# Optimization experiments

Measured on AMD Instinct MI355X. Metric: run time of the kernel, lower is better.

The kernel has to match this reference:

```python
import jax, jax.numpy as jnp
import numpy as np

B, T, C, H = 2, 2048, 1024, 16
HD = C // H  # head dim = 64


def setup_inputs() -> dict:
    key = jax.random.key(0)
    k1, k2, k3 = jax.random.split(key, 3)
    x = jax.random.normal(k1, (B, T, C), dtype=jnp.float32)
    W_attn = jax.random.normal(k2, (C, 3 * C), dtype=jnp.float32) * (C ** -0.5)
    W_proj = jax.random.normal(k3, (C, C), dtype=jnp.float32) * (C ** -0.5)
    b_proj = jnp.zeros((C,), dtype=jnp.float32)
    return {"x": x, "W_attn": W_attn, "W_proj": W_proj, "b_proj": b_proj}


def reference(x, W_attn, W_proj, b_proj):
    Bv, Tv, Cv = x.shape
    qkv = x @ W_attn  # [B, T, 3C]  (no bias: config.bias=False)
    # NOTE: source splits as k, q, v (k first!)
    k, q, v = jnp.split(qkv, 3, axis=2)
    # [B, H, T, HD]
    q = q.reshape(Bv, Tv, H, HD).transpose(0, 2, 1, 3)
    k = k.reshape(Bv, Tv, H, HD).transpose(0, 2, 1, 3)
    v = v.reshape(Bv, Tv, H, HD).transpose(0, 2, 1, 3)
    wei = jnp.einsum('bhqd,bhkd->bhqk', q, k) * (HD ** -0.5)
    causal = jnp.tril(jnp.ones((Tv, Tv), dtype=bool))
    wei = jnp.where(causal, wei, -jnp.inf)
    wei = jax.nn.softmax(wei, axis=-1)
    # dropout = 0.0 (eval) -> identity
    out = jnp.einsum('bhqk,bhkd->bhqd', wei, v)
    out = out.transpose(0, 2, 1, 3).reshape(Bv, Tv, Cv)
    out = out @ W_proj + b_proj
    return out
```

## Files before the change

kernel.cpp:

```cpp
#include <hip/hip_runtime.h>

typedef __attribute__((ext_vector_type(8))) short short8;
typedef __attribute__((ext_vector_type(4))) short short4v;
typedef __attribute__((ext_vector_type(4))) float float4v;

#define T_SEQ 2048
#define CDIM 1024
#define NHEAD 16
#define HDIM 64
#define PROW 72

__device__ __forceinline__ unsigned short f2bf(float f) {
    unsigned u = __builtin_bit_cast(unsigned, f);
    u += 0x7FFF + ((u >> 16) & 1);
    return (unsigned short)(u >> 16);
}

__device__ __forceinline__ void gload16(const unsigned short* g,
                                        unsigned short* l) {
    __builtin_amdgcn_global_load_lds(
        (const __attribute__((address_space(1))) unsigned int*)g,
        (__attribute__((address_space(3))) unsigned int*)l, 16, 0, 0);
}

__device__ __forceinline__ void phase_barrier() {
    __builtin_amdgcn_sched_barrier(0);
    __builtin_amdgcn_s_barrier();
    __builtin_amdgcn_sched_barrier(0);
}

__global__ __launch_bounds__(256) void preproc(
    const float* __restrict__ x, unsigned short* __restrict__ xb,
    const float* __restrict__ Wa, unsigned short* __restrict__ WaT,
    const float* __restrict__ Wp, unsigned short* __restrict__ WpT) {
    int bid = blockIdx.x, tid = threadIdx.x;
    if (bid < 4096) {
        int i = bid * 256 + tid;
        float4 v = ((const float4*)x)[i];
        ushort4 o;
        o.x = f2bf(v.x); o.y = f2bf(v.y); o.z = f2bf(v.z); o.w = f2bf(v.w);
        ((ushort4*)xb)[i] = o;
        return;
    }
    __shared__ float tile[32][33];
    const float* in;
    unsigned short* out;
    int N, b;
    if (bid < 4096 + 3072) {
        b = bid - 4096; in = Wa; out = WaT; N = 3072;
    } else {
        b = bid - 7168; in = Wp; out = WpT; N = 1024;
    }
    const int K = 1024;
    int kb = (b & 31) * 32, nb = (b >> 5) * 32;
    int tx = tid & 31, ty = tid >> 5;
    for (int r = 0; r < 4; r++)
        tile[ty + r * 8][tx] = in[(size_t)(kb + ty + r * 8) * N + nb + tx];
    __syncthreads();
    for (int r = 0; r < 4; r++)
        out[(size_t)(nb + ty + r * 8) * K + kb + tx] = f2bf(tile[tx][ty + r * 8]);
}

__global__ __launch_bounds__(256) void gemm_qkv(
    const unsigned short* __restrict__ A, const unsigned short* __restrict__ Bt,
    unsigned short* __restrict__ dK, unsigned short* __restrict__ dQ,
    unsigned short* __restrict__ dV) {
    const int K = 1024;
    const int NITER = K / 32;
    __shared__ unsigned short sA[3][128 * 32];
    __shared__ unsigned short sB[3][128 * 32];
    int tid = threadIdx.x, wave = tid >> 6, lane = tid & 63;
    int quad = lane >> 4, l16 = lane & 15;
    int wm = wave >> 1, wn = wave & 1;
    int blockM = blockIdx.y * 128, blockN = blockIdx.x * 128;
    bool swapAB = (blockN >= 2048);

    const unsigned short* gA = A + (size_t)blockM * K;
    const unsigned short* gB = Bt + (size_t)blockN * K;

    int srow = wave * 32 + (lane >> 2);
    int scol = (lane & 3) * 8;
    const unsigned short* pa0 = gA + (size_t)srow * K + scol;
    const unsigned short* pa1 = pa0 + (size_t)16 * K;
    const unsigned short* pb0 = gB + (size_t)srow * K + scol;
    const unsigned short* pb1 = pb0 + (size_t)16 * K;
    int lo0 = (wave * 32) * 32;
    int lo1 = (wave * 32 + 16) * 32;

    float4v acc[4][4] = {};
    int aoff = (wm * 64 + l16) * 32 + quad * 8;
    int boff = (wn * 64 + l16) * 32 + quad * 8;

    for (int t = 0; t < 2; t++) {
        int kb = t * 32;
        gload16(pa0 + kb, sA[t] + lo0);
        gload16(pa1 + kb, sA[t] + lo1);
        gload16(pb0 + kb, sB[t] + lo0);
        gload16(pb1 + kb, sB[t] + lo1);
    }
    asm volatile("s_waitcnt vmcnt(4)" ::: "memory");
    phase_barrier();

#pragma unroll
    for (int it = 0; it < NITER; it++) {
        int cur = it % 3;
        if (it + 2 < NITER) {
            int kb = (it + 2) * 32;
            int nb = (it + 2) % 3;
            gload16(pa0 + kb, sA[nb] + lo0);
            gload16(pa1 + kb, sA[nb] + lo1);
            gload16(pb0 + kb, sB[nb] + lo0);
            gload16(pb1 + kb, sB[nb] + lo1);
        }
        const unsigned short* cA = sA[cur];
        const unsigned short* cB = sB[cur];
        short8 af[4], bf[4];
        for (int i = 0; i < 4; i++)
            af[i] = *(const short8*)(cA + aoff + i * 16 * 32);
        for (int j = 0; j < 4; j++)
            bf[j] = *(const short8*)(cB + boff + j * 16 * 32);
        if (!swapAB) {
            for (int i = 0; i < 4; i++)
                for (int j = 0; j < 4; j++)
                    acc[i][j] = __builtin_amdgcn_mfma_f32_16x16x32_bf16(
                        af[i], bf[j], acc[i][j], 0, 0, 0);
        } else {
            for (int i = 0; i < 4; i++)
                for (int j = 0; j < 4; j++)
                    acc[i][j] = __builtin_amdgcn_mfma_f32_16x16x32_bf16(
                        bf[j], af[i], acc[i][j], 0, 0, 0);
        }
        if (it + 1 < NITER) {
            if (it + 2 < NITER) {
                asm volatile("s_waitcnt vmcnt(4)" ::: "memory");
            } else {
                asm volatile("s_waitcnt vmcnt(0)" ::: "memory");
            }
            phase_barrier();
        }
    }

    if (!swapAB) {
        const float QSCL = 0.18033688011112042f;
        for (int i = 0; i < 4; i++)
            for (int j = 0; j < 4; j++)
                for (int r = 0; r < 4; r++) {
                    int m = blockM + wm * 64 + i * 16 + quad * 4 + r;
                    int n = blockN + wn * 64 + j * 16 + l16;
                    int part = n >> 10, c = n & 1023;
                    int h = c >> 6, d = c & 63;
                    int bb = m >> 11, t = m & 2047;
                    int bh = bb * NHEAD + h;
                    if (part == 0) {
                        dK[(((size_t)bh * T_SEQ + t) << 6) + d] = f2bf(acc[i][j][r]);
                    } else {
                        dQ[(((size_t)bh * T_SEQ + t) << 6) + d] =
                            f2bf(acc[i][j][r] * QSCL);
                    }
                }
    } else {
        for (int i = 0; i < 4; i++)
            for (int j = 0; j < 4; j++)
                for (int r = 0; r < 4; r++) {
                    int n = blockN + wn * 64 + j * 16 + quad * 4 + r;
                    int m = blockM + wm * 64 + i * 16 + l16;
                    int c = n & 1023;
                    int h = c >> 6, d = c & 63;
                    int bb = m >> 11, t = m & 2047;
                    int bh = bb * NHEAD + h;
                    dV[((size_t)bh * HDIM + d) * T_SEQ + t] = f2bf(acc[i][j][r]);
                }
    }
}

__global__ __launch_bounds__(256) void gemm_proj(
    const unsigned short* __restrict__ A, const unsigned short* __restrict__ Bt,
    const float* __restrict__ bias, float* __restrict__ out) {
    const int K = 1024;
    const int NITER = K / 64;
    __shared__ unsigned short sA[2][64 * PROW];
    __shared__ unsigned short sB[2][64 * PROW];
    int tid = threadIdx.x, wave = tid >> 6, lane = tid & 63;
    int quad = lane >> 4, l16 = lane & 15;
    int wm = wave >> 1, wn = wave & 1;
    int blockM = blockIdx.y * 64, blockN = blockIdx.x * 64;

    int srow = tid >> 3;
    int sseg = tid & 7;
    const unsigned short* gA0 = A + (size_t)(blockM + srow) * K + sseg * 8;
    const unsigned short* gA1 = gA0 + (size_t)32 * K;
    const unsigned short* gB0 = Bt + (size_t)(blockN + srow) * K + sseg * 8;
    const unsigned short* gB1 = gB0 + (size_t)32 * K;
    int so0 = srow * PROW + sseg * 8;
    int so1 = (srow + 32) * PROW + sseg * 8;

    float4v acc[2][2] = {};
    uint4 ra0, ra1, rb0, rb1;

    ra0 = *(const uint4*)gA0; ra1 = *(const uint4*)gA1;
    rb0 = *(const uint4*)gB0; rb1 = *(const uint4*)gB1;
    *(uint4*)(sA[0] + so0) = ra0;
    *(uint4*)(sA[0] + so1) = ra1;
    *(uint4*)(sB[0] + so0) = rb0;
    *(uint4*)(sB[0] + so1) = rb1;

    int aoff = (wm * 32 + l16) * PROW + quad * 8;
    int boff = (wn * 32 + l16) * PROW + quad * 8;

    for (int it = 0; it < NITER; it++) {
        int cur = it & 1;
        __syncthreads();
        if (it + 1 < NITER) {
            int kb = (it + 1) * 64;
            ra0 = *(const uint4*)(gA0 + kb); ra1 = *(const uint4*)(gA1 + kb);
            rb0 = *(const uint4*)(gB0 + kb); rb1 = *(const uint4*)(gB1 + kb);
        }
        const unsigned short* cA = sA[cur];
        const unsigned short* cB = sB[cur];
        short8 af[2][2], bf[2][2];
        for (int i = 0; i < 2; i++)
            for (int k = 0; k < 2; k++)
                af[i][k] = *(const short8*)(cA + aoff + i * 16 * PROW + k * 32);
        for (int j = 0; j < 2; j++)
            for (int k = 0; k < 2; k++)
                bf[j][k] = *(const short8*)(cB + boff + j * 16 * PROW + k * 32);
        for (int i = 0; i < 2; i++)
            for (int j = 0; j < 2; j++) {
                acc[i][j] = __builtin_amdgcn_mfma_f32_16x16x32_bf16(
                    af[i][0], bf[j][0], acc[i][j], 0, 0, 0);
                acc[i][j] = __builtin_amdgcn_mfma_f32_16x16x32_bf16(
                    af[i][1], bf[j][1], acc[i][j], 0, 0, 0);
            }
        if (it + 1 < NITER) {
            int nxt = cur ^ 1;
            *(uint4*)(sA[nxt] + so0) = ra0;
            *(uint4*)(sA[nxt] + so1) = ra1;
            *(uint4*)(sB[nxt] + so0) = rb0;
            *(uint4*)(sB[nxt] + so1) = rb1;
        }
    }

    for (int i = 0; i < 2; i++)
        for (int j = 0; j < 2; j++)
            for (int r = 0; r < 4; r++) {
                int m = blockM + wm * 32 + i * 16 + quad * 4 + r;
                int n = blockN + wn * 32 + j * 16 + l16;
                out[(size_t)m * CDIM + n] = acc[i][j][r] + bias[n];
            }
}

__global__ __launch_bounds__(256) void attn_fwd(
    const unsigned short* __restrict__ Qp, const unsigned short* __restrict__ Kp,
    const unsigned short* __restrict__ Vt, unsigned short* __restrict__ att) {
    __shared__ unsigned short sK[2][64 * 72];
    __shared__ unsigned short sV[2][64 * 72];
    int tid = threadIdx.x, wave = tid >> 6, lane = tid & 63;
    int quad = lane >> 4, l16 = lane & 15;
    int bh = blockIdx.x;
    int bb = bh >> 4, h = bh & 15;
    size_t baseQ = (size_t)bh * T_SEQ * HDIM;
    size_t baseV = (size_t)bh * HDIM * T_SEQ;
    int row4 = tid >> 2, seg = tid & 3;

    int xt = 31 - blockIdx.y;
    int qb = xt * 64;
    int qrow = qb + wave * 16 + l16;

    const unsigned short* qr = Qp + baseQ + (size_t)qrow * HDIM;
    short8 qf0 = *(const short8*)(qr + quad * 8);
    short8 qf1 = *(const short8*)(qr + 32 + quad * 8);

    float4v o[4] = {};
    float lsum = 0.f;
    int nt = xt + 1;

    uint4 ka, kb2, va, vb;
    {
        const unsigned short* gk = Kp + baseQ + (size_t)row4 * HDIM + seg * 16;
        const unsigned short* gv = Vt + baseV + (size_t)row4 * T_SEQ + seg * 16;
        ka = *(const uint4*)gk; kb2 = *(const uint4*)(gk + 8);
        va = *(const uint4*)gv; vb = *(const uint4*)(gv + 8);
    }
    *(uint4*)(sK[0] + row4 * 72 + seg * 16) = ka;
    *(uint4*)(sK[0] + row4 * 72 + seg * 16 + 8) = kb2;
    *(uint4*)(sV[0] + row4 * 72 + seg * 16) = va;
    *(uint4*)(sV[0] + row4 * 72 + seg * 16 + 8) = vb;

    for (int t = 0; t < nt; t++) {
        int cur = t & 1;
        __syncthreads();
        if (t + 1 < nt) {
            const unsigned short* gk =
                Kp + baseQ + (size_t)((t + 1) * 64 + row4) * HDIM + seg * 16;
            const unsigned short* gv =
                Vt + baseV + (size_t)row4 * T_SEQ + (t + 1) * 64 + seg * 16;
            ka = *(const uint4*)gk; kb2 = *(const uint4*)(gk + 8);
            va = *(const uint4*)gv; vb = *(const uint4*)(gv + 8);
        }

        const unsigned short* cK = sK[cur];
        const unsigned short* cV = sV[cur];
        float4v s[4];
        for (int sub = 0; sub < 4; sub++) {
            short8 kf0 = *(const short8*)(cK + (sub * 16 + l16) * 72 + quad * 8);
            short8 kf1 =
                *(const short8*)(cK + (sub * 16 + l16) * 72 + 32 + quad * 8);
            float4v z = {};
            z = __builtin_amdgcn_mfma_f32_16x16x32_bf16(kf0, qf0, z, 0, 0, 0);
            z = __builtin_amdgcn_mfma_f32_16x16x32_bf16(kf1, qf1, z, 0, 0, 0);
            s[sub] = z;
        }

        bool need_mask = (t * 64 + 63) > (qb + wave * 16);
        float p[16];
        for (int sub = 0; sub < 4; sub++)
            for (int r = 0; r < 4; r++) {
                float v = s[sub][r];
                if (need_mask) {
                    int kg = t * 64 + sub * 16 + quad * 4 + r;
                    v = (kg <= qrow) ? v : -1e30f;
                }
                p[sub * 4 + r] = v;
            }
        unsigned ub[16];
        for (int i = 0; i < 16; i++) {
            float e = exp2f(p[i] - 16.0f);
            unsigned u = __builtin_bit_cast(unsigned, e) & 0xffff0000u;
            ub[i] = u;
            lsum += __builtin_bit_cast(float, u);
        }

        for (int sub = 0; sub < 4; sub++) {
            unsigned lo = __builtin_amdgcn_perm(ub[sub * 4 + 1], ub[sub * 4 + 0],
                                                0x07060302u);
            unsigned hi = __builtin_amdgcn_perm(ub[sub * 4 + 3], ub[sub * 4 + 2],
                                                0x07060302u);
            uint2 packed = {lo, hi};
            short4v pf = __builtin_bit_cast(short4v, packed);
            for (int dc = 0; dc < 4; dc++) {
                short4v vf = *(const short4v*)(
                    cV + (dc * 16 + l16) * 72 + sub * 16 + quad * 4);
                o[dc] = __builtin_amdgcn_mfma_f32_16x16x16bf16_1k(
                    vf, pf, o[dc], 0, 0, 0);
            }
        }

        if (t + 1 < nt) {
            int nxt = cur ^ 1;
            *(uint4*)(sK[nxt] + row4 * 72 + seg * 16) = ka;
            *(uint4*)(sK[nxt] + row4 * 72 + seg * 16 + 8) = kb2;
            *(uint4*)(sV[nxt] + row4 * 72 + seg * 16) = va;
            *(uint4*)(sV[nxt] + row4 * 72 + seg * 16 + 8) = vb;
        }
    }

    lsum += __shfl_xor(lsum, 16);
    lsum += __shfl_xor(lsum, 32);
    float inv = 1.0f / lsum;

    __syncthreads();
    for (int dc = 0; dc < 4; dc++) {
        short4v ov;
        for (int r = 0; r < 4; r++) ov[r] = (short)f2bf(o[dc][r] * inv);
        *(short4v*)(sK[0] + wave * 1152 + l16 * 72 + dc * 16 + quad * 4) = ov;
    }
    __syncthreads();
    int orow = lane >> 2, oseg = lane & 3;
    uint4 a = *(const uint4*)(sK[0] + wave * 1152 + orow * 72 + oseg * 16);
    uint4 b = *(const uint4*)(sK[0] + wave * 1152 + orow * 72 + oseg * 16 + 8);
    unsigned short* dst = att +
        (size_t)(bb * T_SEQ + qb + wave * 16 + orow) * CDIM + h * HDIM +
        oseg * 16;
    *(uint4*)dst = a;
    *(uint4*)(dst + 8) = b;
}

extern "C" void kernel_launch(void* const* d_in, const int* in_sizes, int n_in,
                              void* d_out, int out_size, void* d_ws, size_t ws_size,
                              hipStream_t stream) {
    const float* x      = (const float*)d_in[0];
    const float* W_attn = (const float*)d_in[1];
    const float* W_proj = (const float*)d_in[2];
    const float* b_proj = (const float*)d_in[3];
    float* out = (float*)d_out;

    unsigned short* xb   = (unsigned short*)d_ws;
    unsigned short* WaT  = xb  + 4096 * 1024;
    unsigned short* WpT  = WaT + 3072 * 1024;
    unsigned short* Karr = WpT + 1024 * 1024;
    unsigned short* Qarr = Karr + 2 * 16 * 2048 * 64;
    unsigned short* Varr = Qarr + 2 * 16 * 2048 * 64;
    unsigned short* attb = Varr + 2 * 16 * 2048 * 64;

    preproc<<<8192, 256, 0, stream>>>(x, xb, W_attn, WaT, W_proj, WpT);
    gemm_qkv<<<dim3(24, 32), 256, 0, stream>>>(xb, WaT, Karr, Qarr, Varr);
    attn_fwd<<<dim3(32, 32), 256, 0, stream>>>(Qarr, Karr, Varr, attb);
    gemm_proj<<<dim3(16, 64), 256, 0, stream>>>(attb, WpT, b_proj, out);
}
```

Baseline: 190.7 us.

## Retile projection GEMM with async triple buffering; streamline attention softmax

The projection GEMM moves from 64x64 tiles with register-staged double buffering to 128x128 tiles. It loads through global_load_lds into three 32-wide K buffers, and explicit vmcnt waits let two stages stay in flight. In the attention kernel the -16 offset is folded into the MFMA accumulator init and the mask is applied after a hardware exp2. The masked and unmasked paths are split, and s_setprio raises priority around the MFMA sections. The larger GEMM tile launches only 256 blocks, which may underfill the GPU. The unpadded 32-wide LDS rows may cause bank conflicts.

```diff
diff --git a/kernel.cpp b/kernel.cpp
--- a/kernel.cpp
+++ b/kernel.cpp
@@ -8,7 +8,6 @@
 #define CDIM 1024
 #define NHEAD 16
 #define HDIM 64
-#define PROW 72
 
 __device__ __forceinline__ unsigned short f2bf(float f) {
     unsigned u = __builtin_bit_cast(unsigned, f);
@@ -177,75 +176,80 @@
     const unsigned short* __restrict__ A, const unsigned short* __restrict__ Bt,
     const float* __restrict__ bias, float* __restrict__ out) {
     const int K = 1024;
-    const int NITER = K / 64;
-    __shared__ unsigned short sA[2][64 * PROW];
-    __shared__ unsigned short sB[2][64 * PROW];
+    const int NITER = K / 32;
+    __shared__ unsigned short sA[3][128 * 32];
+    __shared__ unsigned short sB[3][128 * 32];
     int tid = threadIdx.x, wave = tid >> 6, lane = tid & 63;
     int quad = lane >> 4, l16 = lane & 15;
     int wm = wave >> 1, wn = wave & 1;
-    int blockM = blockIdx.y * 64, blockN = blockIdx.x * 64;
-
-    int srow = tid >> 3;
-    int sseg = tid & 7;
-    const unsigned short* gA0 = A + (size_t)(blockM + srow) * K + sseg * 8;
-    const unsigned short* gA1 = gA0 + (size_t)32 * K;
-    const unsigned short* gB0 = Bt + (size_t)(blockN + srow) * K + sseg * 8;
-    const unsigned short* gB1 = gB0 + (size_t)32 * K;
-    int so0 = srow * PROW + sseg * 8;
-    int so1 = (srow + 32) * PROW + sseg * 8;
-
-    float4v acc[2][2] = {};
-    uint4 ra0, ra1, rb0, rb1;
-
-    ra0 = *(const uint4*)gA0; ra1 = *(const uint4*)gA1;
-    rb0 = *(const uint4*)gB0; rb1 = *(const uint4*)gB1;
-    *(uint4*)(sA[0] + so0) = ra0;
-    *(uint4*)(sA[0] + so1) = ra1;
-    *(uint4*)(sB[0] + so0) = rb0;
-    *(uint4*)(sB[0] + so1) = rb1;
-
-    int aoff = (wm * 32 + l16) * PROW + quad * 8;
-    int boff = (wn * 32 + l16) * PROW + quad * 8;
-
+    int blockM = blockIdx.y * 128, blockN = blockIdx.x * 128;
+
+    const unsigned short* gA = A + (size_t)blockM * K;
+    const unsigned short* gB = Bt + (size_t)blockN * K;
+
+    int srow = wave * 32 + (lane >> 2);
+    int scol = (lane & 3) * 8;
+    const unsigned short* pa0 = gA + (size_t)srow * K + scol;
+    const unsigned short* pa1 = pa0 + (size_t)16 * K;
+    const unsigned short* pb0 = gB + (size_t)srow * K + scol;
+    const unsigned short* pb1 = pb0 + (size_t)16 * K;
+    int lo0 = (wave * 32) * 32;
+    int lo1 = (wave * 32 + 16) * 32;
+
+    float4v acc[4][4] = {};
+    int aoff = (wm * 64 + l16) * 32 + quad * 8;
+    int boff = (wn * 64 + l16) * 32 + quad * 8;
+
+    for (int t = 0; t < 2; t++) {
+        int kb = t * 32;
+        gload16(pa0 + kb, sA[t] + lo0);
+        gload16(pa1 + kb, sA[t] + lo1);
+        gload16(pb0 + kb, sB[t] + lo0);
+        gload16(pb1 + kb, sB[t] + lo1);
+    }
+    asm volatile("s_waitcnt vmcnt(4)" ::: "memory");
+    phase_barrier();
+
+#pragma unroll
     for (int it = 0; it < NITER; it++) {
-        int cur = it & 1;
-        __syncthreads();
-        if (it + 1 < NITER) {
-            int kb = (it + 1) * 64;
-            ra0 = *(const uint4*)(gA0 + kb); ra1 = *(const uint4*)(gA1 + kb);
-            rb0 = *(const uint4*)(gB0 + kb); rb1 = *(const uint4*)(gB1 + kb);
+        int cur = it % 3;
+        if (it + 2 < NITER) {
+            int kb = (it + 2) * 32;
+            int nb = (it + 2) % 3;
+            gload16(pa0 + kb, sA[nb] + lo0);
+            gload16(pa1 + kb, sA[nb] + lo1);
+            gload16(pb0 + kb, sB[nb] + lo0);
+            gload16(pb1 + kb, sB[nb] + lo1);
         }
         const unsigned short* cA = sA[cur];
         const unsigned short* cB = sB[cur];
-        short8 af[2][2], bf[2][2];
-        for (int i = 0; i < 2; i++)
-            for (int k = 0; k < 2; k++)
-                af[i][k] = *(const short8*)(cA + aoff + i * 16 * PROW + k * 32);
-        for (int j = 0; j < 2; j++)
-            for (int k = 0; k < 2; k++)
-                bf[j][k] = *(const short8*)(cB + boff + j * 16 * PROW + k * 32);
-        for (int i = 0; i < 2; i++)
-            for (int j = 0; j < 2; j++) {
+        short8 af[4], bf[4];
+        for (int i = 0; i < 4; i++)
+            af[i] = *(const short8*)(cA + aoff + i * 16 * 32);
+        for (int j = 0; j < 4; j++)
+            bf[j] = *(const short8*)(cB + boff + j * 16 * 32);
+        for (int i = 0; i < 4; i++)
+            for (int j = 0; j < 4; j++)
                 acc[i][j] = __builtin_amdgcn_mfma_f32_16x16x32_bf16(
-                    af[i][0], bf[j][0], acc[i][j], 0, 0, 0);
-                acc[i][j] = __builtin_amdgcn_mfma_f32_16x16x32_bf16(
-                    af[i][1], bf[j][1], acc[i][j], 0, 0, 0);
+                    af[i], bf[j], acc[i][j], 0, 0, 0);
+        if (it + 1 < NITER) {
+            if (it + 2 < NITER) {
+                asm volatile("s_waitcnt vmcnt(4)" ::: "memory");
+            } else {
+                asm volatile("s_waitcnt vmcnt(0)" ::: "memory");
             }
-        if (it + 1 < NITER) {
-            int nxt = cur ^ 1;
-            *(uint4*)(sA[nxt] + so0) = ra0;
-            *(uint4*)(sA[nxt] + so1) = ra1;
-            *(uint4*)(sB[nxt] + so0) = rb0;
-            *(uint4*)(sB[nxt] + so1) = rb1;
-        }
-    }
-
-    for (int i = 0; i < 2; i++)
-        for (int j = 0; j < 2; j++)
+            phase_barrier();
+        }
+    }
+
+    float bv[4];
+    for (int j = 0; j < 4; j++) bv[j] = bias[blockN + wn * 64 + j * 16 + l16];
+    for (int i = 0; i < 4; i++)
+        for (int j = 0; j < 4; j++)
             for (int r = 0; r < 4; r++) {
-                int m = blockM + wm * 32 + i * 16 + quad * 4 + r;
-                int n = blockN + wn * 32 + j * 16 + l16;
-                out[(size_t)m * CDIM + n] = acc[i][j][r] + bias[n];
+                int m = blockM + wm * 64 + i * 16 + quad * 4 + r;
+                int n = blockN + wn * 64 + j * 16 + l16;
+                out[(size_t)m * CDIM + n] = acc[i][j][r] + bv[j];
             }
 }
 
@@ -286,6 +290,8 @@
     *(uint4*)(sV[0] + row4 * 72 + seg * 16) = va;
     *(uint4*)(sV[0] + row4 * 72 + seg * 16 + 8) = vb;
 
+    const float4v NEG16 = {-16.f, -16.f, -16.f, -16.f};
+
     for (int t = 0; t < nt; t++) {
         int cur = t & 1;
         __syncthreads();
@@ -301,35 +307,41 @@
         const unsigned short* cK = sK[cur];
         const unsigned short* cV = sV[cur];
         float4v s[4];
+        __builtin_amdgcn_s_setprio(1);
         for (int sub = 0; sub < 4; sub++) {
             short8 kf0 = *(const short8*)(cK + (sub * 16 + l16) * 72 + quad * 8);
             short8 kf1 =
                 *(const short8*)(cK + (sub * 16 + l16) * 72 + 32 + quad * 8);
-            float4v z = {};
+            float4v z = NEG16;
             z = __builtin_amdgcn_mfma_f32_16x16x32_bf16(kf0, qf0, z, 0, 0, 0);
             z = __builtin_amdgcn_mfma_f32_16x16x32_bf16(kf1, qf1, z, 0, 0, 0);
             s[sub] = z;
         }
-
+        __builtin_amdgcn_s_setprio(0);
+
+        unsigned ub[16];
         bool need_mask = (t * 64 + 63) > (qb + wave * 16);
-        float p[16];
-        for (int sub = 0; sub < 4; sub++)
-            for (int r = 0; r < 4; r++) {
-                float v = s[sub][r];
-                if (need_mask) {
-                    int kg = t * 64 + sub * 16 + quad * 4 + r;
-                    v = (kg <= qrow) ? v : -1e30f;
+        if (need_mask) {
+            int kgb = t * 64 + quad * 4;
+            for (int sub = 0; sub < 4; sub++)
+                for (int r = 0; r < 4; r++) {
+                    float e = __builtin_amdgcn_exp2f(s[sub][r]);
+                    e = (kgb + sub * 16 + r <= qrow) ? e : 0.0f;
+                    unsigned u = __builtin_bit_cast(unsigned, e) & 0xffff0000u;
+                    ub[sub * 4 + r] = u;
+                    lsum += __builtin_bit_cast(float, u);
                 }
-                p[sub * 4 + r] = v;
-            }
-        unsigned ub[16];
-        for (int i = 0; i < 16; i++) {
-            float e = exp2f(p[i] - 16.0f);
-            unsigned u = __builtin_bit_cast(unsigned, e) & 0xffff0000u;
-            ub[i] = u;
-            lsum += __builtin_bit_cast(float, u);
-        }
-
+        } else {
+            for (int sub = 0; sub < 4; sub++)
+                for (int r = 0; r < 4; r++) {
+                    float e = __builtin_amdgcn_exp2f(s[sub][r]);
+                    unsigned u = __builtin_bit_cast(unsigned, e) & 0xffff0000u;
+                    ub[sub * 4 + r] = u;
+                    lsum += __builtin_bit_cast(float, u);
+                }
+        }
+
+        __builtin_amdgcn_s_setprio(1);
         for (int sub = 0; sub < 4; sub++) {
             unsigned lo = __builtin_amdgcn_perm(ub[sub * 4 + 1], ub[sub * 4 + 0],
                                                 0x07060302u);
@@ -344,6 +356,7 @@
                     vf, pf, o[dc], 0, 0, 0);
             }
         }
+        __builtin_amdgcn_s_setprio(0);
 
         if (t + 1 < nt) {
             int nxt = cur ^ 1;
@@ -395,5 +408,5 @@
     preproc<<<8192, 256, 0, stream>>>(x, xb, W_attn, WaT, W_proj, WpT);
     gemm_qkv<<<dim3(24, 32), 256, 0, stream>>>(xb, WaT, Karr, Qarr, Varr);
     attn_fwd<<<dim3(32, 32), 256, 0, stream>>>(Qarr, Karr, Varr, attb);
-    gemm_proj<<<dim3(16, 64), 256, 0, stream>>>(attb, WpT, b_proj, out);
-}
+    gemm_proj<<<dim3(8, 32), 256, 0, stream>>>(attb, WpT, b_proj, out);
+}
```

New measurement: 196.0 us. 1.03x slower.
